# Performance work log

Hardware: AMD Instinct MI355X
Metric: run time of the kernel (lower is better)

## Reference

```python
import jax, jax.numpy as jnp
import numpy as np

B, N = 64, 1024
DIMS = [1, 32, 64, 64, 1]   # dim after insert(0,1) and append(1)
DEGS = [2, 2, 2, 2]
EPS = 1e-5


def setup_inputs() -> dict:
    key = jax.random.key(0)
    ks = jax.random.split(key, 16)
    inp = {
        "e": jax.random.uniform(ks[0], (B, N), jnp.float32),
        "phi": jax.random.normal(ks[1], (B, N), jnp.float32),
        "eta": jax.random.normal(ks[2], (B, N), jnp.float32),
    }
    for i in range(4):
        fan_in = DIMS[i] * DEGS[i]
        inp[f"W{i}"] = jax.random.normal(ks[3 + 2 * i], (DIMS[i + 1], fan_in), jnp.float32) / np.sqrt(fan_in)
        inp[f"b{i}"] = jnp.zeros((DIMS[i + 1],), jnp.float32)
    return inp


def _gconv(adj, x, W, b, deg):
    # x: [B, C, N], adj: [B, N, N]
    # operators: [x, x@A, x@A^2, ...] up to deg powers (A^0 = identity)
    ops = [x]
    for _ in range(deg - 1):
        ops.append(jnp.einsum('bcn,bnm->bcm', ops[-1], adj))
    cat = jnp.concatenate(ops, axis=1)                 # [B, C*deg, N]
    return jnp.einsum('oc,bcn->bon', W, cat) + b[None, :, None]


def reference(e, phi, eta, W0, b0, W1, b1, W2, b2, W3, b3):
    # batchnorm(e, axis=1): standardize each event over its particles
    mu = e.mean(axis=1, keepdims=True)
    sd = e.std(axis=1, keepdims=True)
    e = (e - mu) / (sd + EPS)
    e = e[:, None, :]                                   # [B, 1, N]

    # Adjacency: gaussian kernel of squared euclidean distance in (phi, eta)
    d2 = (phi[:, :, None] - phi[:, None, :]) ** 2 + (eta[:, :, None] - eta[:, None, :]) ** 2
    adj = jnp.exp(-d2)                                  # [B, N, N]

    Ws = (W0, W1, W2, W3)
    bs = (b0, b1, b2, b3)
    for i in range(3):
        e = jax.nn.relu(_gconv(adj, e, Ws[i], bs[i], DEGS[i]))
    e = _gconv(adj, e, Ws[3], bs[3], DEGS[3])           # [B, 1, N]

    out = e.mean(axis=2)[:, 0]                          # [B], + logistic_bias (=0)
    return jax.nn.sigmoid(out)
```

## Files before the change

### kernel.cpp

```cpp
#include <hip/hip_runtime.h>
#include <hip/hip_bf16.h>
#include <math.h>

#define BB 64
#define NN 1024
#define EPSV 1e-5f

typedef unsigned short u16;
typedef __attribute__((ext_vector_type(8))) short short8;
typedef __attribute__((ext_vector_type(4))) float f32x4;

#define GLOBAL_AS __attribute__((address_space(1)))
#define LDS_AS __attribute__((address_space(3)))

#define SCL 1.20112240878645f

static __device__ __forceinline__ void gload_lds16(const void* g, void* l) {
  __builtin_amdgcn_global_load_lds((const GLOBAL_AS unsigned int*)g,
                                   (LDS_AS unsigned int*)l, 16, 0, 0);
}

static __device__ __forceinline__ u16 f2bf(float f) {
  __hip_bfloat16 h = __float2bfloat16(f);
  union { __hip_bfloat16 h; u16 s; } u; u.h = h; return u.s;
}
static __device__ __forceinline__ float bf2f(u16 s) {
  unsigned int u = ((unsigned int)s) << 16;
  union { unsigned int u; float f; } c; c.u = u; return c.f;
}
static __device__ __forceinline__ float expn2(float dp, float de) {
#if __has_builtin(__builtin_amdgcn_exp2f)
  return __builtin_amdgcn_exp2f(fmaf(-dp, dp, -(de * de)));
#else
  return exp2f(fmaf(-dp, dp, -(de * de)));
#endif
}

template<int N>
static __device__ __forceinline__ void wait_vm() {
  static_assert(N == 0 || N == 1 || N == 2 || N == 4, "");
  if constexpr (N == 0) asm volatile("s_waitcnt vmcnt(0)" ::: "memory");
  if constexpr (N == 1) asm volatile("s_waitcnt vmcnt(1)" ::: "memory");
  if constexpr (N == 2) asm volatile("s_waitcnt vmcnt(2)" ::: "memory");
  if constexpr (N == 4) asm volatile("s_waitcnt vmcnt(4)" ::: "memory");
}

static __device__ __forceinline__ void remap(int L, int& b, int& bx) {
  b = (L & 7) * 8 + (L >> 7);
  bx = (L >> 3) & 15;
}

__global__ __launch_bounds__(256, 4) void fused0_kernel(
    const float* __restrict__ e,
    const float* __restrict__ phi, const float* __restrict__ eta,
    const float* __restrict__ W0, const float* __restrict__ b0,
    const float* __restrict__ W1, const float* __restrict__ W2,
    u16* __restrict__ Wp1, u16* __restrict__ Wp2,
    u16* __restrict__ ZN,
    u16* __restrict__ XT)
{
  __shared__ float x0[NN];
  __shared__ float2 pe[NN];
  __shared__ float red[256];
  __shared__ u16 zt[64 * 40];

  int b, bx;
  remap(blockIdx.x, b, bx);
  int m0 = bx * 64;
  int tid = threadIdx.x;

  if (bx == 0 && b == 0)
    for (int i = tid; i < 64 * 64; i += 256) Wp1[i] = f2bf(W1[i]);
  if (bx == 0 && b == 1)
    for (int i = tid; i < 64 * 128; i += 256) Wp2[i] = f2bf(W2[i]);

  const float* er = e + (size_t)b * NN;
  const float* phb = phi + (size_t)b * NN;
  const float* etb = eta + (size_t)b * NN;

  float s = 0.f;
  for (int i = tid; i < NN; i += 256) {
    float v = er[i]; x0[i] = v; s += v;
    pe[i] = make_float2(phb[i] * SCL, etb[i] * SCL);
  }
  red[tid] = s; __syncthreads();
  for (int off = 128; off > 0; off >>= 1) {
    if (tid < off) red[tid] += red[tid + off];
    __syncthreads();
  }
  float mu = red[0] * (1.f / NN);
  __syncthreads();
  float s2 = 0.f;
  for (int i = tid; i < NN; i += 256) { float d = x0[i] - mu; s2 += d * d; }
  red[tid] = s2; __syncthreads();
  for (int off = 128; off > 0; off >>= 1) {
    if (tid < off) red[tid] += red[tid + off];
    __syncthreads();
  }
  float sd = sqrtf(red[0] * (1.f / NN));
  float inv = 1.f / (sd + EPSV);
  for (int i = tid; i < NN; i += 256) x0[i] = (x0[i] - mu) * inv;
  __syncthreads();

  int q = tid >> 6;
  int mi = tid & 63;
  int m = m0 + mi;
  float phm = pe[m].x, etm = pe[m].y;

  const float2* pp = &pe[q * 256];
  const float* xx = &x0[q * 256];
  float t0a = 0.f, t0b = 0.f;
#pragma unroll 4
  for (int n = 0; n < 256; n += 2) {
    float2 qa = pp[n], qb = pp[n + 1];
    float dpa = qa.x - phm, dea = qa.y - etm;
    float dpb = qb.x - phm, deb = qb.y - etm;
    t0a = fmaf(expn2(dpa, dea), xx[n], t0a);
    t0b = fmaf(expn2(dpb, deb), xx[n + 1], t0b);
  }
  red[q * 64 + mi] = t0a + t0b;
  __syncthreads();
  float t0 = (red[0 * 64 + mi] + red[1 * 64 + mi]) +
             (red[2 * 64 + mi] + red[3 * 64 + mi]);

  float x0m = x0[m];
  union { short8 v; u16 h[8]; } zrow;
#pragma unroll
  for (int oj = 0; oj < 8; ++oj) {
    int o = q * 8 + oj;
    float z = fmaf(W0[o * 2], x0m, fmaf(W0[o * 2 + 1], t0, b0[o]));
    zrow.h[oj] = f2bf(fmaxf(z, 0.f));
  }
  *(short8*)&ZN[((size_t)b * NN + m) * 32 + q * 8] = zrow.v;
  *(short8*)&zt[mi * 40 + q * 8] = zrow.v;
  __syncthreads();
  size_t basew = ((size_t)b * (NN / 8) + (m0 >> 3)) * (size_t)(32 * 8);
  for (int flat = tid; flat < 64 * 32; flat += 256) {
    int mo = flat >> 8;
    int o  = (flat >> 3) & 31;
    int m8 = flat & 7;
    XT[basew + flat] = zt[(mo * 8 + m8) * 40 + o];
  }
}

template<int CE, int O>
__global__ __launch_bounds__(256, 4) void fused_kernel(
    const u16* __restrict__ XT,
    const u16* __restrict__ XN,
    const float* __restrict__ phi,
    const float* __restrict__ eta,
    const u16* __restrict__ Wp,
    const float* __restrict__ bias,
    u16* __restrict__ ZN,
    u16* __restrict__ XTo)
{
  constexpr int NT = 128;
  constexpr int NCT = CE / 16;
  constexpr int SLAB = NT * CE;
  constexpr int SLABV = SLAB / 8;
  constexpr int LPT = SLABV / 256;
  constexpr int KW = 2 * CE;
  constexpr int S = KW + 8;
  constexpr int OT = O / 16;
  constexpr int KS = KW / 32;
  constexpr int STEPS = NN / NT;
  constexpr int KCN = NT / 32;

  constexpr int PH1 = (int)sizeof(float2) * NN + 2 * SLAB * 2;
  constexpr int PH2 = 64 * S * 2;
  constexpr int ZTS = 64 * (O + 8) * 2;
  constexpr int SM0 = PH1 > PH2 ? PH1 : PH2;
  constexpr int SM = SM0 > ZTS ? SM0 : ZTS;
  __shared__ __align__(16) char smem[SM];
  float2* pe = (float2*)smem;
  u16* slabB = (u16*)(smem + sizeof(float2) * NN);
  u16* cat = (u16*)smem;
  u16* zt  = (u16*)smem;

  int b, bx;
  remap(blockIdx.x, b, bx);
  int m0 = bx * 64;
  int tid = threadIdx.x;
  int lane = tid & 63, w = tid >> 6, g = lane >> 4, cl = lane & 15;

  const float* phb = phi + (size_t)b * NN;
  const float* etb = eta + (size_t)b * NN;
  for (int i = tid; i < NN; i += 256)
    pe[i] = make_float2(phb[i] * SCL, etb[i] * SCL);

  int m_lane = m0 + w * 16 + cl;
  float phm = phb[m_lane] * SCL;
  float etm = etb[m_lane] * SCL;

  f32x4 acc[NCT];
#pragma unroll
  for (int ci = 0; ci < NCT; ++ci) acc[ci] = (f32x4){0.f, 0.f, 0.f, 0.f};

  const u16* xtb = XT + (size_t)b * NN * CE;

  auto stage = [&](int step, u16* dst) {
#pragma unroll
    for (int k = 0; k < LPT; ++k) {
      int v = tid + k * 256;
      int gg = v / CE, cc = v % CE;
      int cs = cc ^ (gg & 7);
      gload_lds16(xtb + ((size_t)((step * NT >> 3) + gg) * CE + cs) * 8,
                  dst + v * 8);
    }
  };

  stage(0, slabB);
  __syncthreads();

  for (int s = 0; s < STEPS; ++s) {
    union { short8 v[KCN]; u16 h[KCN][8]; } af;
#pragma unroll
    for (int kc = 0; kc < KCN; ++kc) {
      const float2* pp = &pe[s * NT + kc * 32 + 8 * g];
#pragma unroll
      for (int j = 0; j < 8; ++j) {
        float2 qq = pp[j];
        af.h[kc][j] = f2bf(expn2(qq.x - phm, qq.y - etm));
      }
    }
    __builtin_amdgcn_sched_barrier(0);
    __builtin_amdgcn_s_barrier();
    __builtin_amdgcn_sched_barrier(0);
    if (s + 1 < STEPS) {
      stage(s + 1, slabB + ((s + 1) & 1) * SLAB);
      wait_vm<LPT>();
    } else {
      wait_vm<0>();
    }
    __builtin_amdgcn_sched_barrier(0);

    const u16* cur = slabB + (s & 1) * SLAB;
#pragma unroll
    for (int kc = 0; kc < KCN; ++kc) {
      int ggr = kc * 4 + g, sw = ggr & 7;
#pragma unroll
      for (int ci = 0; ci < NCT; ++ci) {
        const short8* bp =
            (const short8*)&cur[(ggr * CE + ((ci * 16 + cl) ^ sw)) * 8];
        acc[ci] = __builtin_amdgcn_mfma_f32_16x16x32_bf16(af.v[kc], *bp, acc[ci], 0, 0, 0);
      }
    }
  }
  __syncthreads();

  constexpr int CV = CE / 8;
  constexpr int NXN = (64 * CV + 255) / 256;
  constexpr bool XFULL = (64 * CV) % 256 == 0;
  short8 xnr[NXN];
#pragma unroll
  for (int i = 0; i < NXN; ++i) {
    int v = tid + i * 256;
    if (XFULL || v < 64 * CV) {
      int m = v / CV, cv = v % CV;
      xnr[i] = *(const short8*)&XN[((size_t)b * NN + m0 + m) * CE + cv * 8];
    }
  }
  float bz[OT];
#pragma unroll
  for (int oi = 0; oi < OT; ++oi) bz[oi] = bias[oi * 16 + cl];

#pragma unroll
  for (int ci = 0; ci < NCT; ++ci)
#pragma unroll
    for (int r = 0; r < 4; ++r) {
      int m = w * 16 + g * 4 + r;
      cat[m * S + CE + ci * 16 + cl] = f2bf(acc[ci][r]);
    }
#pragma unroll
  for (int i = 0; i < NXN; ++i) {
    int v = tid + i * 256;
    if (XFULL || v < 64 * CV) {
      int m = v / CV, cv = v % CV;
      *(short8*)&cat[m * S + cv * 8] = xnr[i];
    }
  }
  __syncthreads();

  short8 afp[KS];
#pragma unroll
  for (int kk = 0; kk < KS; ++kk)
    afp[kk] = *(const short8*)&cat[(w * 16 + cl) * S + kk * 32 + g * 8];

  constexpr int OB = (8 / KS) < OT ? (8 / KS) : OT;
  f32x4 pacc[OT];
#pragma unroll
  for (int oi = 0; oi < OT; ++oi) pacc[oi] = (f32x4){0.f, 0.f, 0.f, 0.f};
#pragma unroll
  for (int ob = 0; ob < OT; ob += OB) {
    short8 wfr[OB][KS];
#pragma unroll
    for (int oi = 0; oi < OB; ++oi)
#pragma unroll
      for (int kk = 0; kk < KS; ++kk)
        wfr[oi][kk] = *(const short8*)&Wp[((ob + oi) * 16 + cl) * KW + kk * 32 + g * 8];
#pragma unroll
    for (int oi = 0; oi < OB; ++oi)
#pragma unroll
      for (int kk = 0; kk < KS; ++kk)
        pacc[ob + oi] = __builtin_amdgcn_mfma_f32_16x16x32_bf16(
            afp[kk], wfr[oi][kk], pacc[ob + oi], 0, 0, 0);
  }
  __syncthreads();

#pragma unroll
  for (int oi = 0; oi < OT; ++oi) {
#pragma unroll
    for (int r = 0; r < 4; ++r) {
      float z = fmaxf(pacc[oi][r] + bz[oi], 0.f);
      u16 zb = f2bf(z);
      int m = w * 16 + 4 * g + r;
      ZN[((size_t)b * NN + m0 + m) * O + oi * 16 + cl] = zb;
      zt[m * (O + 8) + oi * 16 + cl] = zb;
    }
  }
  __syncthreads();
  size_t basew = ((size_t)b * (NN / 8) + (m0 >> 3)) * (size_t)(O * 8);
  for (int flat = tid; flat < 64 * O; flat += 256) {
    int mo = flat / (O * 8);
    int o  = (flat >> 3) % O;
    int m8 = flat & 7;
    XTo[basew + flat] = zt[(mo * 8 + m8) * (O + 8) + o];
  }
}

__global__ __launch_bounds__(256, 4) void fused_last_kernel(
    const u16* __restrict__ XT,
    const u16* __restrict__ XN,
    const float* __restrict__ phi,
    const float* __restrict__ eta,
    const float* __restrict__ W3,
    const float* __restrict__ b3,
    float* __restrict__ partial)
{
  constexpr int CE = 64, NCT = 4, NT = 128;
  constexpr int SLAB = NT * CE;
  constexpr int SLABV = SLAB / 8;
  constexpr int LPT = SLABV / 256;
  constexpr int S = 136;
  constexpr int STEPS = NN / NT;
  constexpr int KCN = NT / 32;

  constexpr int PH1 = (int)sizeof(float2) * NN + 2 * SLAB * 2;
  __shared__ __align__(16) char smem[PH1];
  float2* pe = (float2*)smem;
  u16* slabB = (u16*)(smem + sizeof(float2) * NN);
  u16* cat = (u16*)smem;
  float* sW = (float*)(smem + 17408);
  float* red = (float*)(smem + 17408 + 512);

  int b, bx;
  remap(blockIdx.x, b, bx);
  int m0 = bx * 64;
  int tid = threadIdx.x;
  int lane = tid & 63, w = tid >> 6, g = lane >> 4, cl = lane & 15;

  const float* phb = phi + (size_t)b * NN;
  const float* etb = eta + (size_t)b * NN;
  for (int i = tid; i < NN; i += 256)
    pe[i] = make_float2(phb[i] * SCL, etb[i] * SCL);

  int m_lane = m0 + w * 16 + cl;
  float phm = phb[m_lane] * SCL;
  float etm = etb[m_lane] * SCL;

  f32x4 acc[NCT];
#pragma unroll
  for (int ci = 0; ci < NCT; ++ci) acc[ci] = (f32x4){0.f, 0.f, 0.f, 0.f};

  const u16* xtb = XT + (size_t)b * NN * CE;

  auto stage = [&](int step, u16* dst) {
#pragma unroll
    for (int k = 0; k < LPT; ++k) {
      int v = tid + k * 256;
      int gg = v / CE, cc = v % CE;
      int cs = cc ^ (gg & 7);
      gload_lds16(xtb + ((size_t)((step * NT >> 3) + gg) * CE + cs) * 8,
                  dst + v * 8);
    }
  };

  stage(0, slabB);
  __syncthreads();

  for (int s = 0; s < STEPS; ++s) {
    union { short8 v[KCN]; u16 h[KCN][8]; } af;
#pragma unroll
    for (int kc = 0; kc < KCN; ++kc) {
      const float2* pp = &pe[s * NT + kc * 32 + 8 * g];
#pragma unroll
      for (int j = 0; j < 8; ++j) {
        float2 qq = pp[j];
        af.h[kc][j] = f2bf(expn2(qq.x - phm, qq.y - etm));
      }
    }
    __builtin_amdgcn_sched_barrier(0);
    __builtin_amdgcn_s_barrier();
    __builtin_amdgcn_sched_barrier(0);
    if (s + 1 < STEPS) {
      stage(s + 1, slabB + ((s + 1) & 1) * SLAB);
      wait_vm<LPT>();
    } else {
      wait_vm<0>();
    }
    __builtin_amdgcn_sched_barrier(0);

    const u16* cur = slabB + (s & 1) * SLAB;
#pragma unroll
    for (int kc = 0; kc < KCN; ++kc) {
      int ggr = kc * 4 + g, sw = ggr & 7;
#pragma unroll
      for (int ci = 0; ci < NCT; ++ci) {
        const short8* bp =
            (const short8*)&cur[(ggr * CE + ((ci * 16 + cl) ^ sw)) * 8];
        acc[ci] = __builtin_amdgcn_mfma_f32_16x16x32_bf16(af.v[kc], *bp, acc[ci], 0, 0, 0);
      }
    }
  }
  __syncthreads();

  short8 xnr0, xnr1;
  {
    int v0 = tid, v1 = tid + 256;
    int ma = v0 >> 3, ca = v0 & 7, mb = v1 >> 3, cb = v1 & 7;
    xnr0 = *(const short8*)&XN[((size_t)b * NN + m0 + ma) * CE + ca * 8];
    xnr1 = *(const short8*)&XN[((size_t)b * NN + m0 + mb) * CE + cb * 8];
  }
  if (tid < 128) sW[tid] = W3[tid];
#pragma unroll
  for (int ci = 0; ci < NCT; ++ci)
#pragma unroll
    for (int r = 0; r < 4; ++r) {
      int m = w * 16 + g * 4 + r;
      cat[m * S + CE + ci * 16 + cl] = f2bf(acc[ci][r]);
    }
  {
    int v0 = tid, v1 = tid + 256;
    int ma = v0 >> 3, ca = v0 & 7, mb = v1 >> 3, cb = v1 & 7;
    *(short8*)&cat[ma * S + ca * 8] = xnr0;
    *(short8*)&cat[mb * S + cb * 8] = xnr1;
  }
  __syncthreads();

  int m = tid & 63, q = tid >> 6;
  float sacc = 0.f;
#pragma unroll
  for (int v = 0; v < 4; ++v) {
    short8 cv = *(const short8*)&cat[m * S + q * 32 + v * 8];
#pragma unroll
    for (int j = 0; j < 8; ++j)
      sacc = fmaf(sW[q * 32 + v * 8 + j], bf2f((u16)cv[j]), sacc);
  }
  red[tid] = sacc; __syncthreads();
  for (int off = 128; off > 0; off >>= 1) {
    if (tid < off) red[tid] += red[tid + off];
    __syncthreads();
  }
  if (tid == 0)
    partial[b * 16 + bx] = red[0] + 64.f * b3[0];
}

__global__ __launch_bounds__(64) void final_kernel(const float* __restrict__ partial,
                                                   float* __restrict__ out) {
  int b = blockIdx.x;
  int lane = threadIdx.x;
  float v = (lane < 16) ? partial[b * 16 + lane] : 0.f;
#pragma unroll
  for (int off = 8; off > 0; off >>= 1) v += __shfl_down(v, off);
  if (lane == 0) out[b] = 1.f / (1.f + __expf(-(v * (1.f / NN))));
}

extern "C" void kernel_launch(void* const* d_in, const int* in_sizes, int n_in,
                              void* d_out, int out_size, void* d_ws, size_t ws_size,
                              hipStream_t stream) {
  const float* e   = (const float*)d_in[0];
  const float* phi = (const float*)d_in[1];
  const float* eta = (const float*)d_in[2];
  const float* W0  = (const float*)d_in[3];
  const float* b0  = (const float*)d_in[4];
  const float* W1  = (const float*)d_in[5];
  const float* b1  = (const float*)d_in[6];
  const float* W2  = (const float*)d_in[7];
  const float* b2  = (const float*)d_in[8];
  const float* W3  = (const float*)d_in[9];
  const float* b3  = (const float*)d_in[10];

  char* wsb = (char*)d_ws;
  const size_t MB = 1u << 20;
  float* PB = (float*)(wsb);
  u16* XT1 = (u16*)(wsb + 4 * MB);
  u16* XN1 = (u16*)(wsb + 8 * MB);
  u16* XT2 = (u16*)(wsb + 12 * MB);
  u16* XN2 = (u16*)(wsb + 20 * MB);
  u16* XT3 = (u16*)(wsb + 28 * MB);
  u16* XN3 = (u16*)(wsb + 36 * MB);
  u16* Wp1 = (u16*)(wsb + 44 * MB);
  u16* Wp2 = Wp1 + 64 * 64;

  dim3 blk(256);
  dim3 gg(1024);

  fused0_kernel<<<gg, blk, 0, stream>>>(e, phi, eta, W0, b0, W1, W2,
                                        Wp1, Wp2, XN1, XT1);
  fused_kernel<32, 64><<<gg, blk, 0, stream>>>(XT1, XN1, phi, eta, Wp1, b1, XN2, XT2);
  fused_kernel<64, 64><<<gg, blk, 0, stream>>>(XT2, XN2, phi, eta, Wp2, b2, XN3, XT3);
  fused_last_kernel<<<gg, blk, 0, stream>>>(XT3, XN3, phi, eta, W3, b3, PB);

  final_kernel<<<BB, dim3(64), 0, stream>>>(PB, (float*)d_out);
}
```

Before: 93.77 us.

## Halve block size so each wave computes two row tiles sharing B fragments

The fused layer kernels now launch 128-thread blocks, and each wave computes two 16-row tiles (A and B) of the 64-row output block instead of one. Each LDS-loaded B fragment of the adjacency-times-features MFMA feeds two MFMAs, which halves LDS reads per MFMA, and the staging loads per thread double. The change raises register pressure from doubled accumulators and per-thread exp work, and leaves fewer waves per block to hide latency.

```diff
diff --git a/kernel.cpp b/kernel.cpp
--- a/kernel.cpp
+++ b/kernel.cpp
@@ -38,11 +38,12 @@
 
 template<int N>
 static __device__ __forceinline__ void wait_vm() {
-  static_assert(N == 0 || N == 1 || N == 2 || N == 4, "");
+  static_assert(N == 0 || N == 1 || N == 2 || N == 4 || N == 8, "");
   if constexpr (N == 0) asm volatile("s_waitcnt vmcnt(0)" ::: "memory");
   if constexpr (N == 1) asm volatile("s_waitcnt vmcnt(1)" ::: "memory");
   if constexpr (N == 2) asm volatile("s_waitcnt vmcnt(2)" ::: "memory");
   if constexpr (N == 4) asm volatile("s_waitcnt vmcnt(4)" ::: "memory");
+  if constexpr (N == 8) asm volatile("s_waitcnt vmcnt(8)" ::: "memory");
 }
 
 static __device__ __forceinline__ void remap(int L, int& b, int& bx) {
@@ -144,7 +145,7 @@
 }
 
 template<int CE, int O>
-__global__ __launch_bounds__(256, 4) void fused_kernel(
+__global__ __launch_bounds__(128, 2) void fused_kernel(
     const u16* __restrict__ XT,
     const u16* __restrict__ XN,
     const float* __restrict__ phi,
@@ -158,7 +159,7 @@
   constexpr int NCT = CE / 16;
   constexpr int SLAB = NT * CE;
   constexpr int SLABV = SLAB / 8;
-  constexpr int LPT = SLABV / 256;
+  constexpr int LPT = SLABV / 128;
   constexpr int KW = 2 * CE;
   constexpr int S = KW + 8;
   constexpr int OT = O / 16;
@@ -185,23 +186,27 @@
 
   const float* phb = phi + (size_t)b * NN;
   const float* etb = eta + (size_t)b * NN;
-  for (int i = tid; i < NN; i += 256)
+  for (int i = tid; i < NN; i += 128)
     pe[i] = make_float2(phb[i] * SCL, etb[i] * SCL);
 
-  int m_lane = m0 + w * 16 + cl;
-  float phm = phb[m_lane] * SCL;
-  float etm = etb[m_lane] * SCL;
-
-  f32x4 acc[NCT];
-#pragma unroll
-  for (int ci = 0; ci < NCT; ++ci) acc[ci] = (f32x4){0.f, 0.f, 0.f, 0.f};
+  int mA = m0 + w * 16 + cl;
+  int mB = m0 + 32 + w * 16 + cl;
+  float phmA = phb[mA] * SCL, etmA = etb[mA] * SCL;
+  float phmB = phb[mB] * SCL, etmB = etb[mB] * SCL;
+
+  f32x4 accA[NCT], accB[NCT];
+#pragma unroll
+  for (int ci = 0; ci < NCT; ++ci) {
+    accA[ci] = (f32x4){0.f, 0.f, 0.f, 0.f};
+    accB[ci] = (f32x4){0.f, 0.f, 0.f, 0.f};
+  }
 
   const u16* xtb = XT + (size_t)b * NN * CE;
 
   auto stage = [&](int step, u16* dst) {
 #pragma unroll
     for (int k = 0; k < LPT; ++k) {
-      int v = tid + k * 256;
+      int v = tid + k * 128;
       int gg = v / CE, cc = v % CE;
       int cs = cc ^ (gg & 7);
       gload_lds16(xtb + ((size_t)((step * NT >> 3) + gg) * CE + cs) * 8,
@@ -213,14 +218,15 @@
   __syncthreads();
 
   for (int s = 0; s < STEPS; ++s) {
-    union { short8 v[KCN]; u16 h[KCN][8]; } af;
+    union { short8 v[KCN]; u16 h[KCN][8]; } afA, afB;
 #pragma unroll
     for (int kc = 0; kc < KCN; ++kc) {
       const float2* pp = &pe[s * NT + kc * 32 + 8 * g];
 #pragma unroll
       for (int j = 0; j < 8; ++j) {
         float2 qq = pp[j];
-        af.h[kc][j] = f2bf(expn2(qq.x - phm, qq.y - etm));
+        afA.h[kc][j] = f2bf(expn2(qq.x - phmA, qq.y - etmA));
+        afB.h[kc][j] = f2bf(expn2(qq.x - phmB, qq.y - etmB));
       }
     }
     __builtin_amdgcn_sched_barrier(0);
@@ -240,25 +246,22 @@
       int ggr = kc * 4 + g, sw = ggr & 7;
 #pragma unroll
       for (int ci = 0; ci < NCT; ++ci) {
-        const short8* bp =
-            (const short8*)&cur[(ggr * CE + ((ci * 16 + cl) ^ sw)) * 8];
-        acc[ci] = __builtin_amdgcn_mfma_f32_16x16x32_bf16(af.v[kc], *bp, acc[ci], 0, 0, 0);
+        short8 bp = *(const short8*)&cur[(ggr * CE + ((ci * 16 + cl) ^ sw)) * 8];
+        accA[ci] = __builtin_amdgcn_mfma_f32_16x16x32_bf16(afA.v[kc], bp, accA[ci], 0, 0, 0);
+        accB[ci] = __builtin_amdgcn_mfma_f32_16x16x32_bf16(afB.v[kc], bp, accB[ci], 0, 0, 0);
       }
     }
   }
   __syncthreads();
 
   constexpr int CV = CE / 8;
-  constexpr int NXN = (64 * CV + 255) / 256;
-  constexpr bool XFULL = (64 * CV) % 256 == 0;
+  constexpr int NXN = (64 * CV) / 128;
   short8 xnr[NXN];
 #pragma unroll
   for (int i = 0; i < NXN; ++i) {
-    int v = tid + i * 256;
-    if (XFULL || v < 64 * CV) {
-      int m = v / CV, cv = v % CV;
-      xnr[i] = *(const short8*)&XN[((size_t)b * NN + m0 + m) * CE + cv * 8];
-    }
+    int v = tid + i * 128;
+    int m = v / CV, cv = v % CV;
+    xnr[i] = *(const short8*)&XN[((size_t)b * NN + m0 + m) * CE + cv * 8];
   }
   float bz[OT];
 #pragma unroll
@@ -268,28 +271,32 @@
   for (int ci = 0; ci < NCT; ++ci)
 #pragma unroll
     for (int r = 0; r < 4; ++r) {
-      int m = w * 16 + g * 4 + r;
-      cat[m * S + CE + ci * 16 + cl] = f2bf(acc[ci][r]);
+      int ma = w * 16 + g * 4 + r;
+      cat[ma * S + CE + ci * 16 + cl] = f2bf(accA[ci][r]);
+      cat[(32 + ma) * S + CE + ci * 16 + cl] = f2bf(accB[ci][r]);
     }
 #pragma unroll
   for (int i = 0; i < NXN; ++i) {
-    int v = tid + i * 256;
-    if (XFULL || v < 64 * CV) {
-      int m = v / CV, cv = v % CV;
-      *(short8*)&cat[m * S + cv * 8] = xnr[i];
-    }
-  }
-  __syncthreads();
-
-  short8 afp[KS];
-#pragma unroll
-  for (int kk = 0; kk < KS; ++kk)
-    afp[kk] = *(const short8*)&cat[(w * 16 + cl) * S + kk * 32 + g * 8];
+    int v = tid + i * 128;
+    int m = v / CV, cv = v % CV;
+    *(short8*)&cat[m * S + cv * 8] = xnr[i];
+  }
+  __syncthreads();
+
+  short8 afpA[KS], afpB[KS];
+#pragma unroll
+  for (int kk = 0; kk < KS; ++kk) {
+    afpA[kk] = *(const short8*)&cat[(w * 16 + cl) * S + kk * 32 + g * 8];
+    afpB[kk] = *(const short8*)&cat[(32 + w * 16 + cl) * S + kk * 32 + g * 8];
+  }
 
   constexpr int OB = (8 / KS) < OT ? (8 / KS) : OT;
-  f32x4 pacc[OT];
-#pragma unroll
-  for (int oi = 0; oi < OT; ++oi) pacc[oi] = (f32x4){0.f, 0.f, 0.f, 0.f};
+  f32x4 paccA[OT], paccB[OT];
+#pragma unroll
+  for (int oi = 0; oi < OT; ++oi) {
+    paccA[oi] = (f32x4){0.f, 0.f, 0.f, 0.f};
+    paccB[oi] = (f32x4){0.f, 0.f, 0.f, 0.f};
+  }
 #pragma unroll
   for (int ob = 0; ob < OT; ob += OB) {
     short8 wfr[OB][KS];
@@ -301,9 +308,12 @@
 #pragma unroll
     for (int oi = 0; oi < OB; ++oi)
 #pragma unroll
-      for (int kk = 0; kk < KS; ++kk)
-        pacc[ob + oi] = __builtin_amdgcn_mfma_f32_16x16x32_bf16(
-            afp[kk], wfr[oi][kk], pacc[ob + oi], 0, 0, 0);
+      for (int kk = 0; kk < KS; ++kk) {
+        paccA[ob + oi] = __builtin_amdgcn_mfma_f32_16x16x32_bf16(
+            afpA[kk], wfr[oi][kk], paccA[ob + oi], 0, 0, 0);
+        paccB[ob + oi] = __builtin_amdgcn_mfma_f32_16x16x32_bf16(
+            afpB[kk], wfr[oi][kk], paccB[ob + oi], 0, 0, 0);
+      }
   }
   __syncthreads();
 
@@ -311,16 +321,19 @@
   for (int oi = 0; oi < OT; ++oi) {
 #pragma unroll
     for (int r = 0; r < 4; ++r) {
-      float z = fmaxf(pacc[oi][r] + bz[oi], 0.f);
-      u16 zb = f2bf(z);
-      int m = w * 16 + 4 * g + r;
-      ZN[((size_t)b * NN + m0 + m) * O + oi * 16 + cl] = zb;
-      zt[m * (O + 8) + oi * 16 + cl] = zb;
+      int ma = w * 16 + 4 * g + r;
+      float zA = fmaxf(paccA[oi][r] + bz[oi], 0.f);
+      float zB = fmaxf(paccB[oi][r] + bz[oi], 0.f);
+      u16 zbA = f2bf(zA), zbB = f2bf(zB);
+      ZN[((size_t)b * NN + m0 + ma) * O + oi * 16 + cl] = zbA;
+      ZN[((size_t)b * NN + m0 + 32 + ma) * O + oi * 16 + cl] = zbB;
+      zt[ma * (O + 8) + oi * 16 + cl] = zbA;
+      zt[(32 + ma) * (O + 8) + oi * 16 + cl] = zbB;
     }
   }
   __syncthreads();
   size_t basew = ((size_t)b * (NN / 8) + (m0 >> 3)) * (size_t)(O * 8);
-  for (int flat = tid; flat < 64 * O; flat += 256) {
+  for (int flat = tid; flat < 64 * O; flat += 128) {
     int mo = flat / (O * 8);
     int o  = (flat >> 3) % O;
     int m8 = flat & 7;
@@ -328,7 +341,7 @@
   }
 }
 
-__global__ __launch_bounds__(256, 4) void fused_last_kernel(
+__global__ __launch_bounds__(128, 2) void fused_last_kernel(
     const u16* __restrict__ XT,
     const u16* __restrict__ XN,
     const float* __restrict__ phi,
@@ -340,7 +353,7 @@
   constexpr int CE = 64, NCT = 4, NT = 128;
   constexpr int SLAB = NT * CE;
   constexpr int SLABV = SLAB / 8;
-  constexpr int LPT = SLABV / 256;
+  constexpr int LPT = SLABV / 128;
   constexpr int S = 136;
   constexpr int STEPS = NN / NT;
   constexpr int KCN = NT / 32;
@@ -361,23 +374,27 @@
 
   const float* phb = phi + (size_t)b * NN;
   const float* etb = eta + (size_t)b * NN;
-  for (int i = tid; i < NN; i += 256)
+  for (int i = tid; i < NN; i += 128)
     pe[i] = make_float2(phb[i] * SCL, etb[i] * SCL);
 
-  int m_lane = m0 + w * 16 + cl;
-  float phm = phb[m_lane] * SCL;
-  float etm = etb[m_lane] * SCL;
-
-  f32x4 acc[NCT];
-#pragma unroll
-  for (int ci = 0; ci < NCT; ++ci) acc[ci] = (f32x4){0.f, 0.f, 0.f, 0.f};
+  int mA = m0 + w * 16 + cl;
+  int mB = m0 + 32 + w * 16 + cl;
+  float phmA = phb[mA] * SCL, etmA = etb[mA] * SCL;
+  float phmB = phb[mB] * SCL, etmB = etb[mB] * SCL;
+
+  f32x4 accA[NCT], accB[NCT];
+#pragma unroll
+  for (int ci = 0; ci < NCT; ++ci) {
+    accA[ci] = (f32x4){0.f, 0.f, 0.f, 0.f};
+    accB[ci] = (f32x4){0.f, 0.f, 0.f, 0.f};
+  }
 
   const u16* xtb = XT + (size_t)b * NN * CE;
 
   auto stage = [&](int step, u16* dst) {
 #pragma unroll
     for (int k = 0; k < LPT; ++k) {
-      int v = tid + k * 256;
+      int v = tid + k * 128;
       int gg = v / CE, cc = v % CE;
       int cs = cc ^ (gg & 7);
       gload_lds16(xtb + ((size_t)((step * NT >> 3) + gg) * CE + cs) * 8,
@@ -389,14 +406,15 @@
   __syncthreads();
 
   for (int s = 0; s < STEPS; ++s) {
-    union { short8 v[KCN]; u16 h[KCN][8]; } af;
+    union { short8 v[KCN]; u16 h[KCN][8]; } afA, afB;
 #pragma unroll
     for (int kc = 0; kc < KCN; ++kc) {
       const float2* pp = &pe[s * NT + kc * 32 + 8 * g];
 #pragma unroll
       for (int j = 0; j < 8; ++j) {
         float2 qq = pp[j];
-        af.h[kc][j] = f2bf(expn2(qq.x - phm, qq.y - etm));
+        afA.h[kc][j] = f2bf(expn2(qq.x - phmA, qq.y - etmA));
+        afB.h[kc][j] = f2bf(expn2(qq.x - phmB, qq.y - etmB));
       }
     }
     __builtin_amdgcn_sched_barrier(0);
@@ -416,48 +434,49 @@
       int ggr = kc * 4 + g, sw = ggr & 7;
 #pragma unroll
       for (int ci = 0; ci < NCT; ++ci) {
-        const short8* bp =
-            (const short8*)&cur[(ggr * CE + ((ci * 16 + cl) ^ sw)) * 8];
-        acc[ci] = __builtin_amdgcn_mfma_f32_16x16x32_bf16(af.v[kc], *bp, acc[ci], 0, 0, 0);
+        short8 bp = *(const short8*)&cur[(ggr * CE + ((ci * 16 + cl) ^ sw)) * 8];
+        accA[ci] = __builtin_amdgcn_mfma_f32_16x16x32_bf16(afA.v[kc], bp, accA[ci], 0, 0, 0);
+        accB[ci] = __builtin_amdgcn_mfma_f32_16x16x32_bf16(afB.v[kc], bp, accB[ci], 0, 0, 0);
       }
     }
   }
   __syncthreads();
 
-  short8 xnr0, xnr1;
-  {
-    int v0 = tid, v1 = tid + 256;
-    int ma = v0 >> 3, ca = v0 & 7, mb = v1 >> 3, cb = v1 & 7;
-    xnr0 = *(const short8*)&XN[((size_t)b * NN + m0 + ma) * CE + ca * 8];
-    xnr1 = *(const short8*)&XN[((size_t)b * NN + m0 + mb) * CE + cb * 8];
-  }
-  if (tid < 128) sW[tid] = W3[tid];
+  short8 xnr[4];
+#pragma unroll
+  for (int i = 0; i < 4; ++i) {
+    int v = tid + i * 128;
+    int ma = v >> 3, ca = v & 7;
+    xnr[i] = *(const short8*)&XN[((size_t)b * NN + m0 + ma) * CE + ca * 8];
+  }
+  sW[tid] = W3[tid];
 #pragma unroll
   for (int ci = 0; ci < NCT; ++ci)
 #pragma unroll
     for (int r = 0; r < 4; ++r) {
-      int m = w * 16 + g * 4 + r;
-      cat[m * S + CE + ci * 16 + cl] = f2bf(acc[ci][r]);
-    }
-  {
-    int v0 = tid, v1 = tid + 256;
-    int ma = v0 >> 3, ca = v0 & 7, mb = v1 >> 3, cb = v1 & 7;
-    *(short8*)&cat[ma * S + ca * 8] = xnr0;
-    *(short8*)&cat[mb * S + cb * 8] = xnr1;
+      int ma = w * 16 + g * 4 + r;
+      cat[ma * S + CE + ci * 16 + cl] = f2bf(accA[ci][r]);
+      cat[(32 + ma) * S + CE + ci * 16 + cl] = f2bf(accB[ci][r]);
+    }
+#pragma unroll
+  for (int i = 0; i < 4; ++i) {
+    int v = tid + i * 128;
+    int ma = v >> 3, ca = v & 7;
+    *(short8*)&cat[ma * S + ca * 8] = xnr[i];
   }
   __syncthreads();
 
   int m = tid & 63, q = tid >> 6;
   float sacc = 0.f;
 #pragma unroll
-  for (int v = 0; v < 4; ++v) {
-    short8 cv = *(const short8*)&cat[m * S + q * 32 + v * 8];
+  for (int v = 0; v < 8; ++v) {
+    short8 cv = *(const short8*)&cat[m * S + q * 64 + v * 8];
 #pragma unroll
     for (int j = 0; j < 8; ++j)
-      sacc = fmaf(sW[q * 32 + v * 8 + j], bf2f((u16)cv[j]), sacc);
+      sacc = fmaf(sW[q * 64 + v * 8 + j], bf2f((u16)cv[j]), sacc);
   }
   red[tid] = sacc; __syncthreads();
-  for (int off = 128; off > 0; off >>= 1) {
+  for (int off = 64; off > 0; off >>= 1) {
     if (tid < off) red[tid] += red[tid + off];
     __syncthreads();
   }
@@ -502,14 +521,13 @@
   u16* Wp1 = (u16*)(wsb + 44 * MB);
   u16* Wp2 = Wp1 + 64 * 64;
 
-  dim3 blk(256);
   dim3 gg(1024);
 
-  fused0_kernel<<<gg, blk, 0, stream>>>(e, phi, eta, W0, b0, W1, W2,
-                                        Wp1, Wp2, XN1, XT1);
-  fused_kernel<32, 64><<<gg, blk, 0, stream>>>(XT1, XN1, phi, eta, Wp1, b1, XN2, XT2);
-  fused_kernel<64, 64><<<gg, blk, 0, stream>>>(XT2, XN2, phi, eta, Wp2, b2, XN3, XT3);
-  fused_last_kernel<<<gg, blk, 0, stream>>>(XT3, XN3, phi, eta, W3, b3, PB);
+  fused0_kernel<<<gg, dim3(256), 0, stream>>>(e, phi, eta, W0, b0, W1, W2,
+                                              Wp1, Wp2, XN1, XT1);
+  fused_kernel<32, 64><<<gg, dim3(128), 0, stream>>>(XT1, XN1, phi, eta, Wp1, b1, XN2, XT2);
+  fused_kernel<64, 64><<<gg, dim3(128), 0, stream>>>(XT2, XN2, phi, eta, Wp2, b2, XN3, XT3);
+  fused_last_kernel<<<gg, dim3(128), 0, stream>>>(XT3, XN3, phi, eta, W3, b3, PB);
 
   final_kernel<<<BB, dim3(64), 0, stream>>>(PB, (float*)d_out);
 }
```

Measured after the change: 97.17 us. 3.6% more time.

## Fold final reduction into last kernel via atomic counter; enlarge layer-1 N tile

Applied to the files above, without the earlier changes.

Removes the separate final_kernel launch. Each block of the last layer now bumps a per-batch atomic counter, and the last of the 16 blocks sums the partials and writes the sigmoid output. The counter is reset in the first kernel. Separately, the first fused layer (CE=32) now uses a 256-wide N tile instead of 128, giving fewer pipeline steps at the cost of more LDS per block. This saves one launch and its tail latency, and adds atomics and threadfences.

```diff
diff --git a/kernel.cpp b/kernel.cpp
--- a/kernel.cpp
+++ b/kernel.cpp
@@ -56,6 +56,7 @@
     const float* __restrict__ W0, const float* __restrict__ b0,
     const float* __restrict__ W1, const float* __restrict__ W2,
     u16* __restrict__ Wp1, u16* __restrict__ Wp2,
+    int* __restrict__ cnt,
     u16* __restrict__ ZN,
     u16* __restrict__ XT)
 {
@@ -69,6 +70,7 @@
   int m0 = bx * 64;
   int tid = threadIdx.x;
 
+  if (bx == 0 && tid == 0) cnt[b] = 0;
   if (bx == 0 && b == 0)
     for (int i = tid; i < 64 * 64; i += 256) Wp1[i] = f2bf(W1[i]);
   if (bx == 0 && b == 1)
@@ -143,7 +145,7 @@
   }
 }
 
-template<int CE, int O>
+template<int CE, int O, int NT>
 __global__ __launch_bounds__(256, 4) void fused_kernel(
     const u16* __restrict__ XT,
     const u16* __restrict__ XN,
@@ -154,7 +156,6 @@
     u16* __restrict__ ZN,
     u16* __restrict__ XTo)
 {
-  constexpr int NT = 128;
   constexpr int NCT = CE / 16;
   constexpr int SLAB = NT * CE;
   constexpr int SLABV = SLAB / 8;
@@ -335,7 +336,9 @@
     const float* __restrict__ eta,
     const float* __restrict__ W3,
     const float* __restrict__ b3,
-    float* __restrict__ partial)
+    float* __restrict__ partial,
+    int* __restrict__ cnt,
+    float* __restrict__ out)
 {
   constexpr int CE = 64, NCT = 4, NT = 128;
   constexpr int SLAB = NT * CE;
@@ -461,18 +464,21 @@
     if (tid < off) red[tid] += red[tid + off];
     __syncthreads();
   }
-  if (tid == 0)
+  if (tid == 0) {
     partial[b * 16 + bx] = red[0] + 64.f * b3[0];
-}
-
-__global__ __launch_bounds__(64) void final_kernel(const float* __restrict__ partial,
-                                                   float* __restrict__ out) {
-  int b = blockIdx.x;
-  int lane = threadIdx.x;
-  float v = (lane < 16) ? partial[b * 16 + lane] : 0.f;
-#pragma unroll
-  for (int off = 8; off > 0; off >>= 1) v += __shfl_down(v, off);
-  if (lane == 0) out[b] = 1.f / (1.f + __expf(-(v * (1.f / NN))));
+    __threadfence();
+    int old = atomicAdd(&cnt[b], 1);
+    if (old == 15) {
+      __threadfence();
+      float arr[16];
+#pragma unroll
+      for (int i = 0; i < 16; ++i) arr[i] = partial[b * 16 + i];
+#pragma unroll
+      for (int off = 8; off > 0; off >>= 1)
+        for (int i = 0; i < off; ++i) arr[i] += arr[i + off];
+      out[b] = 1.f / (1.f + __expf(-(arr[0] * (1.f / NN))));
+    }
+  }
 }
 
 extern "C" void kernel_launch(void* const* d_in, const int* in_sizes, int n_in,
@@ -492,7 +498,8 @@
 
   char* wsb = (char*)d_ws;
   const size_t MB = 1u << 20;
-  float* PB = (float*)(wsb);
+  float* PB  = (float*)(wsb);
+  int*   CNT = (int*)(wsb + 64 * 1024);
   u16* XT1 = (u16*)(wsb + 4 * MB);
   u16* XN1 = (u16*)(wsb + 8 * MB);
   u16* XT2 = (u16*)(wsb + 12 * MB);
@@ -506,10 +513,9 @@
   dim3 gg(1024);
 
   fused0_kernel<<<gg, blk, 0, stream>>>(e, phi, eta, W0, b0, W1, W2,
-                                        Wp1, Wp2, XN1, XT1);
-  fused_kernel<32, 64><<<gg, blk, 0, stream>>>(XT1, XN1, phi, eta, Wp1, b1, XN2, XT2);
-  fused_kernel<64, 64><<<gg, blk, 0, stream>>>(XT2, XN2, phi, eta, Wp2, b2, XN3, XT3);
-  fused_last_kernel<<<gg, blk, 0, stream>>>(XT3, XN3, phi, eta, W3, b3, PB);
-
-  final_kernel<<<BB, dim3(64), 0, stream>>>(PB, (float*)d_out);
-}
+                                        Wp1, Wp2, CNT, XN1, XT1);
+  fused_kernel<32, 64, 256><<<gg, blk, 0, stream>>>(XT1, XN1, phi, eta, Wp1, b1, XN2, XT2);
+  fused_kernel<64, 64, 128><<<gg, blk, 0, stream>>>(XT2, XN2, phi, eta, Wp2, b2, XN3, XT3);
+  fused_last_kernel<<<gg, blk, 0, stream>>>(XT3, XN3, phi, eta, W3, b3,
+                                            PB, CNT, (float*)d_out);
+}
```

Result: slower. 117.3 us (+25.1%).
